# Optimization experiments

Measured on AMD Instinct MI355X. Metric: run time of the kernel, lower is better.

## Reference

```python
import jax, jax.numpy as jnp
import numpy as np

B = 4096          # batch_size * world_size
D = 256           # embedding dim
TEMP = 0.5        # temperature
EPS = 1e-8        # torch CosineSimilarity eps


def setup_inputs() -> dict:
    key = jax.random.key(0)
    k1, k2 = jax.random.split(key)
    z_i = jax.random.normal(k1, (B, D), dtype=jnp.float32)
    z_j = jax.random.normal(k2, (B, D), dtype=jnp.float32)
    return {"z_i": z_i, "z_j": z_j}


def reference(z_i, z_j):
    N = 2 * B
    z = jnp.concatenate([z_i, z_j], axis=0)                      # [N, D]
    # Cosine similarity: normalize rows (clamped norm like torch eps), then matmul.
    norms = jnp.maximum(jnp.linalg.norm(z, axis=1, keepdims=True), EPS)
    zn = z / norms
    sim = jnp.matmul(zn, zn.T) / TEMP                            # [N, N]
    # Positive pairs: offsets +B and -B from the diagonal.
    pos = jnp.concatenate([jnp.diagonal(sim, B), jnp.diagonal(sim, -B)])  # [N]
    # Cross-entropy with label 0 over [pos, negatives]:
    # logsumexp over {pos} U {negatives} == logsumexp over row excluding the diagonal
    # (the (i, i±B) entries removed by the mask are exactly re-added as the positive).
    neg_inf = jnp.array(-jnp.inf, dtype=sim.dtype)
    sim_nodiag = jnp.where(jnp.eye(N, dtype=bool), neg_inf, sim)
    lse = jax.nn.logsumexp(sim_nodiag, axis=1)                   # [N]
    loss = jnp.sum(lse - pos) / N                                # reduction='sum' then /N
    return loss
```

## Files before the change

### kernel.cpp

```cpp
#include <hip/hip_runtime.h>

#define NROWS 8192
#define DIM   256
#define BHALF 4096
#define NCHUNK 8
#define SCALE 1.69864358f
#define LN2F  0.69314718f

typedef unsigned char u8;
typedef __attribute__((ext_vector_type(4))) float f32x4;
typedef __attribute__((ext_vector_type(4))) int   i32x4;
typedef __attribute__((ext_vector_type(8))) int   i32x8;

__device__ inline void gload_lds16(const void* g, void* l) {
  __builtin_amdgcn_global_load_lds(
      (const __attribute__((address_space(1))) void*)g,
      (__attribute__((address_space(3))) void*)l, 16, 0, 0);
}

__device__ inline float fp8_to_f32(int b) {
  const int e = (b >> 3) & 15, m = b & 7;
  float mag = e ? __builtin_bit_cast(float, ((e + 120) << 23) | (m << 20))
                : (float)m * 0x1p-9f;
  return (b & 128) ? -mag : mag;
}

__global__ __launch_bounds__(256) void nrm_kernel(const float* __restrict__ zi,
                                                  const float* __restrict__ zj,
                                                  u8* __restrict__ zn8,
                                                  float* __restrict__ rowsum,
                                                  float* __restrict__ pos,
                                                  float* __restrict__ diag,
                                                  int* __restrict__ cnt,
                                                  float* __restrict__ out) {
  const int t = threadIdx.x, b = blockIdx.x;
  const int gid = b * 256 + t;
  if (gid < NROWS) rowsum[gid] = 0.f;
  if (gid < 64) cnt[gid] = 0;
  if (gid == 0) out[0] = 0.f;

  const int w = t >> 6, l = t & 63;
#pragma unroll
  for (int q = 0; q < 2; ++q) {
    const int p = b * 8 + w * 2 + q;
    float4 vi = *(const float4*)(zi + (size_t)p * DIM + l * 4);
    float4 vj = *(const float4*)(zj + (size_t)p * DIM + l * 4);
    float ssi = vi.x * vi.x + vi.y * vi.y + vi.z * vi.z + vi.w * vi.w;
    float ssj = vj.x * vj.x + vj.y * vj.y + vj.z * vj.z + vj.w * vj.w;
#pragma unroll
    for (int m = 1; m < 64; m <<= 1) {
      ssi += __shfl_xor(ssi, m);
      ssj += __shfl_xor(ssj, m);
    }
    const float invi = SCALE / fmaxf(sqrtf(ssi), 1e-8f);
    const float invj = SCALE / fmaxf(sqrtf(ssj), 1e-8f);
    int pi = __builtin_amdgcn_cvt_pk_fp8_f32(vi.x * invi, vi.y * invi, 0, false);
    pi = __builtin_amdgcn_cvt_pk_fp8_f32(vi.z * invi, vi.w * invi, pi, true);
    int pj = __builtin_amdgcn_cvt_pk_fp8_f32(vj.x * invj, vj.y * invj, 0, false);
    pj = __builtin_amdgcn_cvt_pk_fp8_f32(vj.z * invj, vj.w * invj, pj, true);
    *(int*)(zn8 + (size_t)p * DIM + l * 4) = pi;
    *(int*)(zn8 + (size_t)(p + BHALF) * DIM + l * 4) = pj;

    float dot = 0.f, di = 0.f, dj = 0.f;
#pragma unroll
    for (int k2 = 0; k2 < 4; ++k2) {
      const float qi = fp8_to_f32((pi >> (8 * k2)) & 255);
      const float qj = fp8_to_f32((pj >> (8 * k2)) & 255);
      dot += qi * qj; di += qi * qi; dj += qj * qj;
    }
#pragma unroll
    for (int m = 1; m < 64; m <<= 1) {
      dot += __shfl_xor(dot, m);
      di  += __shfl_xor(di, m);
      dj  += __shfl_xor(dj, m);
    }
    if      (l == 0) pos[p] = dot * LN2F;
    else if (l == 1) pos[p + BHALF] = dot * LN2F;
    else if (l == 2) diag[p] = di;
    else if (l == 3) diag[p + BHALF] = dj;
  }
}

__global__ __launch_bounds__(256, 2) void sim_kernel(const u8* __restrict__ zn8,
                                                     float* __restrict__ rowsum,
                                                     const float* __restrict__ pos,
                                                     const float* __restrict__ diag,
                                                     int* __restrict__ cnt,
                                                     float* __restrict__ out) {
  __shared__ __align__(16) u8 Bsm[2][128 * DIM];
  __shared__ float plane[2][128];
  __shared__ float wsum[2];
  __shared__ int sfin;

  const int t = threadIdx.x;
  const int w = t >> 6, l = t & 63;
  const int wa = w >> 1, wb = w & 1;
  const int rl = l & 15, kg = l >> 4;

  const int rp = (int)blockIdx.x >> 3;
  const int ch = (int)blockIdx.x & 7;
  const int colbase = ch * 1024;

  int soff[8], doff[8];
#pragma unroll
  for (int i = 0; i < 8; ++i) {
    int c = i * 256 + t;
    int r = c >> 4, cd = c & 15;
    int cs = (cd & 8) | ((cd ^ r) & 7);
    soff[i] = r * DIM + cs * 16;
    doff[i] = (i * 256 + w * 64) * 16;
  }
  auto STAGE = [&](int base_row, u8* dst) {
#pragma unroll
    for (int i = 0; i < 8; ++i)
      gload_lds16(zn8 + (size_t)base_row * DIM + soff[i], dst + doff[i]);
  };
  auto RD2 = [&](const u8* buf, int row, i32x8* dst) {
    const int salt = row & 7;
    const u8* base = buf + row * DIM;
#pragma unroll
    for (int k = 0; k < 2; ++k) {
      i32x4 lo = *(const i32x4*)(base + ((k * 8 + ((kg * 2) ^ salt)) << 4));
      i32x4 hi = *(const i32x4*)(base + ((k * 8 + ((kg * 2 + 1) ^ salt)) << 4));
      dst[k] = __builtin_shufflevector(lo, hi, 0, 1, 2, 3, 4, 5, 6, 7);
    }
  };

  STAGE(rp * 128, &Bsm[0][0]);
  STAGE(colbase, &Bsm[1][0]);
  asm volatile("s_waitcnt vmcnt(8)" ::: "memory");
  __builtin_amdgcn_sched_barrier(0);
  __builtin_amdgcn_s_barrier();
  __builtin_amdgcn_sched_barrier(0);

  i32x8 pb[4][2];
#pragma unroll
  for (int pj = 0; pj < 4; ++pj)
    RD2(&Bsm[0][0], wb * 64 + pj * 16 + rl, pb[pj]);
  asm volatile("s_waitcnt lgkmcnt(0)" ::: "memory");
  __builtin_amdgcn_sched_barrier(0);

  float rsum[4] = {0.f, 0.f, 0.f, 0.f};
  const f32x4 z4 = {0.f, 0.f, 0.f, 0.f};

  auto EPI = [&](const f32x4* a) {
#pragma unroll
    for (int pj = 0; pj < 4; ++pj)
#pragma unroll
      for (int jj = 0; jj < 4; ++jj)
        rsum[pj] += __builtin_amdgcn_exp2f(a[pj][jj]);
  };

#pragma unroll 2
  for (int ti = 0; ti < 8; ++ti) {
    asm volatile("s_waitcnt vmcnt(0)" ::: "memory");
    __builtin_amdgcn_sched_barrier(0);
    __builtin_amdgcn_s_barrier();
    __builtin_amdgcn_sched_barrier(0);

    const u8* Bb = &Bsm[(ti + 1) & 1][0];
    if (ti < 7) STAGE(colbase + (ti + 1) * 128, &Bsm[ti & 1][0]);

    f32x4 acc[2][4];
    i32x8 af[2][2];
    RD2(Bb, wa * 64 + rl, af[0]);
#pragma unroll
    for (int ci = 0; ci < 4; ++ci) {
      if (ci < 3) RD2(Bb, wa * 64 + (ci + 1) * 16 + rl, af[(ci + 1) & 1]);
      if (ci < 3) asm volatile("s_waitcnt lgkmcnt(4)" ::: "memory");
      else        asm volatile("s_waitcnt lgkmcnt(0)" ::: "memory");
      __builtin_amdgcn_sched_barrier(0);

      __builtin_amdgcn_s_setprio(1);
#pragma unroll
      for (int pj = 0; pj < 4; ++pj)
        acc[ci & 1][pj] = __builtin_amdgcn_mfma_scale_f32_16x16x128_f8f6f4(
            af[ci & 1][0], pb[pj][0], z4,
            0, 0, 0, 0x7f7f7f7f, 0, 0x7f7f7f7f);
#pragma unroll
      for (int pj = 0; pj < 4; ++pj)
        acc[ci & 1][pj] = __builtin_amdgcn_mfma_scale_f32_16x16x128_f8f6f4(
            af[ci & 1][1], pb[pj][1], acc[ci & 1][pj],
            0, 0, 0, 0x7f7f7f7f, 0, 0x7f7f7f7f);
      __builtin_amdgcn_s_setprio(0);
      __builtin_amdgcn_sched_barrier(0);

      if (ci > 0) EPI(acc[(ci - 1) & 1]);
    }
    EPI(acc[1]);
  }

#pragma unroll
  for (int pj = 0; pj < 4; ++pj) {
    rsum[pj] += __shfl_xor(rsum[pj], 16);
    rsum[pj] += __shfl_xor(rsum[pj], 32);
  }
  if (kg == 0) {
#pragma unroll
    for (int pj = 0; pj < 4; ++pj)
      plane[wa][wb * 64 + pj * 16 + rl] = rsum[pj];
  }
  __syncthreads();

  if (t < 128)
    atomicAdd(&rowsum[rp * 128 + t], plane[0][t] + plane[1][t]);
  asm volatile("s_waitcnt vmcnt(0)" ::: "memory");
  __syncthreads();
  if (t == 0) sfin = (atomicAdd(&cnt[rp], 1) == NCHUNK - 1);
  __syncthreads();
  if (sfin) {
    float v = 0.f;
    if (t < 128) {
      const int r = rp * 128 + t;
      float s = atomicAdd(&rowsum[r], 0.f);
      v = logf(s - __builtin_amdgcn_exp2f(diag[r])) - pos[r];
    }
#pragma unroll
    for (int m = 1; m < 64; m <<= 1) v += __shfl_xor(v, m);
    if (l == 0 && t < 128) wsum[w] = v;
    __syncthreads();
    if (t == 0) atomicAdd(out, (wsum[0] + wsum[1]) * (1.f / NROWS));
  }
}

extern "C" void kernel_launch(void* const* d_in, const int* in_sizes, int n_in,
                              void* d_out, int out_size, void* d_ws, size_t ws_size,
                              hipStream_t stream) {
  const float* zi = (const float*)d_in[0];
  const float* zj = (const float*)d_in[1];

  u8*    zn8    = (u8*)d_ws;
  float* rowsum = (float*)((char*)d_ws + (size_t)NROWS * DIM);
  float* pos    = (float*)((char*)rowsum + (size_t)NROWS * 4);
  float* diag   = (float*)((char*)pos + (size_t)NROWS * 4);
  int*   cnt    = (int*)((char*)diag + (size_t)NROWS * 4);
  float* out    = (float*)d_out;

  nrm_kernel<<<512, 256, 0, stream>>>(zi, zj, zn8, rowsum, pos, diag, cnt, out);
  sim_kernel<<<64 * NCHUNK, 256, 0, stream>>>(zn8, rowsum, pos, diag, cnt, out);
}
```

Measured before the change: 31.81 us.

## Switch sim kernel to 32x32x64 FP8 MFMA with per-wave full row ownership

Replaces the 16x16x128 scaled FP8 MFMA tiling, where each wave owned a 64x64 quadrant, with 32x32x64 MFMAs. Each wave now owns 32 column rows against all 128 pinned rows, kept in registers as 16 fragments. The exp2 epilogue moves after the full K loop instead of overlapping with the next MFMA group, and the final per-row reduction now sums over four wave planes. This aims for higher MFMA efficiency and fewer LDS reads of the streaming operand, at the cost of more registers (16 pinned fragments plus 64 accumulators) and losing the overlap of epilogue with compute.

```diff
diff --git a/kernel.cpp b/kernel.cpp
--- a/kernel.cpp
+++ b/kernel.cpp
@@ -8,7 +8,7 @@
 #define LN2F  0.69314718f
 
 typedef unsigned char u8;
-typedef __attribute__((ext_vector_type(4))) float f32x4;
+typedef __attribute__((ext_vector_type(16))) float f32x16;
 typedef __attribute__((ext_vector_type(4))) int   i32x4;
 typedef __attribute__((ext_vector_type(8))) int   i32x8;
 
@@ -88,14 +88,13 @@
                                                      int* __restrict__ cnt,
                                                      float* __restrict__ out) {
   __shared__ __align__(16) u8 Bsm[2][128 * DIM];
-  __shared__ float plane[2][128];
+  __shared__ float plane[4][128];
   __shared__ float wsum[2];
   __shared__ int sfin;
 
   const int t = threadIdx.x;
   const int w = t >> 6, l = t & 63;
-  const int wa = w >> 1, wb = w & 1;
-  const int rl = l & 15, kg = l >> 4;
+  const int n31 = l & 31, kh = l >> 5;
 
   const int rp = (int)blockIdx.x >> 3;
   const int ch = (int)blockIdx.x & 7;
@@ -115,15 +114,13 @@
     for (int i = 0; i < 8; ++i)
       gload_lds16(zn8 + (size_t)base_row * DIM + soff[i], dst + doff[i]);
   };
-  auto RD2 = [&](const u8* buf, int row, i32x8* dst) {
+  auto RD32 = [&](const u8* buf, int row, int kk) -> i32x8 {
     const int salt = row & 7;
     const u8* base = buf + row * DIM;
-#pragma unroll
-    for (int k = 0; k < 2; ++k) {
-      i32x4 lo = *(const i32x4*)(base + ((k * 8 + ((kg * 2) ^ salt)) << 4));
-      i32x4 hi = *(const i32x4*)(base + ((k * 8 + ((kg * 2 + 1) ^ salt)) << 4));
-      dst[k] = __builtin_shufflevector(lo, hi, 0, 1, 2, 3, 4, 5, 6, 7);
-    }
+    const int c0 = kk * 4 + kh * 2;
+    i32x4 lo = *(const i32x4*)(base + (((c0 & 8) | ((c0 ^ salt) & 7)) << 4));
+    i32x4 hi = *(const i32x4*)(base + ((((c0 + 1) & 8) | (((c0 + 1) ^ salt) & 7)) << 4));
+    return __builtin_shufflevector(lo, hi, 0, 1, 2, 3, 4, 5, 6, 7);
   };
 
   STAGE(rp * 128, &Bsm[0][0]);
@@ -133,23 +130,16 @@
   __builtin_amdgcn_s_barrier();
   __builtin_amdgcn_sched_barrier(0);
 
-  i32x8 pb[4][2];
+  i32x8 pb[4][4];
 #pragma unroll
   for (int pj = 0; pj < 4; ++pj)
-    RD2(&Bsm[0][0], wb * 64 + pj * 16 + rl, pb[pj]);
+#pragma unroll
+    for (int kk = 0; kk < 4; ++kk)
+      pb[pj][kk] = RD32(&Bsm[0][0], pj * 32 + n31, kk);
   asm volatile("s_waitcnt lgkmcnt(0)" ::: "memory");
   __builtin_amdgcn_sched_barrier(0);
 
   float rsum[4] = {0.f, 0.f, 0.f, 0.f};
-  const f32x4 z4 = {0.f, 0.f, 0.f, 0.f};
-
-  auto EPI = [&](const f32x4* a) {
-#pragma unroll
-    for (int pj = 0; pj < 4; ++pj)
-#pragma unroll
-      for (int jj = 0; jj < 4; ++jj)
-        rsum[pj] += __builtin_amdgcn_exp2f(a[pj][jj]);
-  };
 
 #pragma unroll 2
   for (int ti = 0; ti < 8; ++ti) {
@@ -161,49 +151,58 @@
     const u8* Bb = &Bsm[(ti + 1) & 1][0];
     if (ti < 7) STAGE(colbase + (ti + 1) * 128, &Bsm[ti & 1][0]);
 
-    f32x4 acc[2][4];
-    i32x8 af[2][2];
-    RD2(Bb, wa * 64 + rl, af[0]);
-#pragma unroll
-    for (int ci = 0; ci < 4; ++ci) {
-      if (ci < 3) RD2(Bb, wa * 64 + (ci + 1) * 16 + rl, af[(ci + 1) & 1]);
-      if (ci < 3) asm volatile("s_waitcnt lgkmcnt(4)" ::: "memory");
-      else        asm volatile("s_waitcnt lgkmcnt(0)" ::: "memory");
+    f32x16 acc[4];
+#pragma unroll
+    for (int pj = 0; pj < 4; ++pj) acc[pj] = (f32x16)(0.f);
+
+    i32x8 af0 = RD32(Bb, w * 32 + n31, 0);
+    i32x8 af1;
+#pragma unroll
+    for (int kk = 0; kk < 4; ++kk) {
+      if (kk < 3) {
+        i32x8 nxt = RD32(Bb, w * 32 + n31, kk + 1);
+        if (kk & 1) af0 = nxt; else af1 = nxt;
+        asm volatile("s_waitcnt lgkmcnt(2)" ::: "memory");
+      } else {
+        asm volatile("s_waitcnt lgkmcnt(0)" ::: "memory");
+      }
       __builtin_amdgcn_sched_barrier(0);
-
+      const i32x8 a = (kk & 1) ? af1 : af0;
       __builtin_amdgcn_s_setprio(1);
 #pragma unroll
       for (int pj = 0; pj < 4; ++pj)
-        acc[ci & 1][pj] = __builtin_amdgcn_mfma_scale_f32_16x16x128_f8f6f4(
-            af[ci & 1][0], pb[pj][0], z4,
-            0, 0, 0, 0x7f7f7f7f, 0, 0x7f7f7f7f);
-#pragma unroll
-      for (int pj = 0; pj < 4; ++pj)
-        acc[ci & 1][pj] = __builtin_amdgcn_mfma_scale_f32_16x16x128_f8f6f4(
-            af[ci & 1][1], pb[pj][1], acc[ci & 1][pj],
-            0, 0, 0, 0x7f7f7f7f, 0, 0x7f7f7f7f);
+        acc[pj] = __builtin_amdgcn_mfma_scale_f32_32x32x64_f8f6f4(
+            a, pb[pj][kk], acc[pj],
+            0, 0,
+            0, 0x7f7f7f7f,
+            0, 0x7f7f7f7f);
       __builtin_amdgcn_s_setprio(0);
-      __builtin_amdgcn_sched_barrier(0);
-
-      if (ci > 0) EPI(acc[(ci - 1) & 1]);
-    }
-    EPI(acc[1]);
+    }
+
+#pragma unroll
+    for (int pj = 0; pj < 4; ++pj) {
+      float e0 = 0.f, e1 = 0.f, e2 = 0.f, e3 = 0.f;
+#pragma unroll
+      for (int r16 = 0; r16 < 16; r16 += 4) {
+        e0 += __builtin_amdgcn_exp2f(acc[pj][r16]);
+        e1 += __builtin_amdgcn_exp2f(acc[pj][r16 + 1]);
+        e2 += __builtin_amdgcn_exp2f(acc[pj][r16 + 2]);
+        e3 += __builtin_amdgcn_exp2f(acc[pj][r16 + 3]);
+      }
+      rsum[pj] += (e0 + e1) + (e2 + e3);
+    }
   }
 
 #pragma unroll
   for (int pj = 0; pj < 4; ++pj) {
-    rsum[pj] += __shfl_xor(rsum[pj], 16);
     rsum[pj] += __shfl_xor(rsum[pj], 32);
-  }
-  if (kg == 0) {
-#pragma unroll
-    for (int pj = 0; pj < 4; ++pj)
-      plane[wa][wb * 64 + pj * 16 + rl] = rsum[pj];
+    if (l < 32) plane[w][pj * 32 + l] = rsum[pj];
   }
   __syncthreads();
 
   if (t < 128)
-    atomicAdd(&rowsum[rp * 128 + t], plane[0][t] + plane[1][t]);
+    atomicAdd(&rowsum[rp * 128 + t],
+              (plane[0][t] + plane[1][t]) + (plane[2][t] + plane[3][t]));
   asm volatile("s_waitcnt vmcnt(0)" ::: "memory");
   __syncthreads();
   if (t == 0) sfin = (atomicAdd(&cnt[rp], 1) == NCHUNK - 1);
```

Result: no change. 31.71 us (-0.3%).

## Drop LDS staging; load column fragments directly from global into registers

Applied to the files above, without the earlier changes.

The sim kernel no longer stages 128-row tiles into shared memory with global_load_lds and barriers. Each wave now reads its MFMA operand fragments straight from global memory (L2/L1) into registers and prefetches the next tile's fragment right after issuing the current MFMAs. This removes the LDS traffic, the swizzle and the per-tile block barriers. The cost is redundant global loads across waves, more VGPRs for the prefetch buffers, and exposed global latency that only the register double-buffering covers.

```diff
diff --git a/kernel.cpp b/kernel.cpp
--- a/kernel.cpp
+++ b/kernel.cpp
@@ -11,12 +11,6 @@
 typedef __attribute__((ext_vector_type(4))) float f32x4;
 typedef __attribute__((ext_vector_type(4))) int   i32x4;
 typedef __attribute__((ext_vector_type(8))) int   i32x8;
-
-__device__ inline void gload_lds16(const void* g, void* l) {
-  __builtin_amdgcn_global_load_lds(
-      (const __attribute__((address_space(1))) void*)g,
-      (__attribute__((address_space(3))) void*)l, 16, 0, 0);
-}
 
 __device__ inline float fp8_to_f32(int b) {
   const int e = (b >> 3) & 15, m = b & 7;
@@ -87,7 +81,6 @@
                                                      const float* __restrict__ diag,
                                                      int* __restrict__ cnt,
                                                      float* __restrict__ out) {
-  __shared__ __align__(16) u8 Bsm[2][128 * DIM];
   __shared__ float plane[2][128];
   __shared__ float wsum[2];
   __shared__ int sfin;
@@ -101,93 +94,64 @@
   const int ch = (int)blockIdx.x & 7;
   const int colbase = ch * 1024;
 
-  int soff[8], doff[8];
-#pragma unroll
-  for (int i = 0; i < 8; ++i) {
-    int c = i * 256 + t;
-    int r = c >> 4, cd = c & 15;
-    int cs = (cd & 8) | ((cd ^ r) & 7);
-    soff[i] = r * DIM + cs * 16;
-    doff[i] = (i * 256 + w * 64) * 16;
-  }
-  auto STAGE = [&](int base_row, u8* dst) {
-#pragma unroll
-    for (int i = 0; i < 8; ++i)
-      gload_lds16(zn8 + (size_t)base_row * DIM + soff[i], dst + doff[i]);
+  auto GRD = [&](int row, i32x4* s) {
+    const u8* base = zn8 + (size_t)row * DIM + kg * 32;
+    s[0] = *(const i32x4*)(base);
+    s[1] = *(const i32x4*)(base + 16);
+    s[2] = *(const i32x4*)(base + 128);
+    s[3] = *(const i32x4*)(base + 144);
   };
-  auto RD2 = [&](const u8* buf, int row, i32x8* dst) {
-    const int salt = row & 7;
-    const u8* base = buf + row * DIM;
-#pragma unroll
-    for (int k = 0; k < 2; ++k) {
-      i32x4 lo = *(const i32x4*)(base + ((k * 8 + ((kg * 2) ^ salt)) << 4));
-      i32x4 hi = *(const i32x4*)(base + ((k * 8 + ((kg * 2 + 1) ^ salt)) << 4));
-      dst[k] = __builtin_shufflevector(lo, hi, 0, 1, 2, 3, 4, 5, 6, 7);
-    }
-  };
-
-  STAGE(rp * 128, &Bsm[0][0]);
-  STAGE(colbase, &Bsm[1][0]);
-  asm volatile("s_waitcnt vmcnt(8)" ::: "memory");
+
+  i32x4 pt[4][4];
+#pragma unroll
+  for (int pj = 0; pj < 4; ++pj)
+    GRD(rp * 128 + wb * 64 + pj * 16 + rl, pt[pj]);
+  i32x4 af[4][4];
+#pragma unroll
+  for (int ci = 0; ci < 4; ++ci)
+    GRD(colbase + wa * 64 + ci * 16 + rl, af[ci]);
   __builtin_amdgcn_sched_barrier(0);
-  __builtin_amdgcn_s_barrier();
-  __builtin_amdgcn_sched_barrier(0);
 
   i32x8 pb[4][2];
 #pragma unroll
-  for (int pj = 0; pj < 4; ++pj)
-    RD2(&Bsm[0][0], wb * 64 + pj * 16 + rl, pb[pj]);
-  asm volatile("s_waitcnt lgkmcnt(0)" ::: "memory");
-  __builtin_amdgcn_sched_barrier(0);
+  for (int pj = 0; pj < 4; ++pj) {
+    pb[pj][0] = __builtin_shufflevector(pt[pj][0], pt[pj][1], 0, 1, 2, 3, 4, 5, 6, 7);
+    pb[pj][1] = __builtin_shufflevector(pt[pj][2], pt[pj][3], 0, 1, 2, 3, 4, 5, 6, 7);
+  }
 
   float rsum[4] = {0.f, 0.f, 0.f, 0.f};
   const f32x4 z4 = {0.f, 0.f, 0.f, 0.f};
 
-  auto EPI = [&](const f32x4* a) {
-#pragma unroll
-    for (int pj = 0; pj < 4; ++pj)
-#pragma unroll
-      for (int jj = 0; jj < 4; ++jj)
-        rsum[pj] += __builtin_amdgcn_exp2f(a[pj][jj]);
-  };
-
 #pragma unroll 2
   for (int ti = 0; ti < 8; ++ti) {
-    asm volatile("s_waitcnt vmcnt(0)" ::: "memory");
-    __builtin_amdgcn_sched_barrier(0);
-    __builtin_amdgcn_s_barrier();
-    __builtin_amdgcn_sched_barrier(0);
-
-    const u8* Bb = &Bsm[(ti + 1) & 1][0];
-    if (ti < 7) STAGE(colbase + (ti + 1) * 128, &Bsm[ti & 1][0]);
-
-    f32x4 acc[2][4];
-    i32x8 af[2][2];
-    RD2(Bb, wa * 64 + rl, af[0]);
+    const int tn = (ti < 7) ? ti + 1 : 7;
+    const int nbase = colbase + tn * 128 + wa * 64 + rl;
+
 #pragma unroll
     for (int ci = 0; ci < 4; ++ci) {
-      if (ci < 3) RD2(Bb, wa * 64 + (ci + 1) * 16 + rl, af[(ci + 1) & 1]);
-      if (ci < 3) asm volatile("s_waitcnt lgkmcnt(4)" ::: "memory");
-      else        asm volatile("s_waitcnt lgkmcnt(0)" ::: "memory");
+      i32x8 a0 = __builtin_shufflevector(af[ci][0], af[ci][1], 0, 1, 2, 3, 4, 5, 6, 7);
+      i32x8 a1 = __builtin_shufflevector(af[ci][2], af[ci][3], 0, 1, 2, 3, 4, 5, 6, 7);
+      f32x4 acc[4];
+      __builtin_amdgcn_s_setprio(1);
+#pragma unroll
+      for (int pj = 0; pj < 4; ++pj)
+        acc[pj] = __builtin_amdgcn_mfma_scale_f32_16x16x128_f8f6f4(
+            a0, pb[pj][0], z4, 0, 0, 0, 0x7f7f7f7f, 0, 0x7f7f7f7f);
+#pragma unroll
+      for (int pj = 0; pj < 4; ++pj)
+        acc[pj] = __builtin_amdgcn_mfma_scale_f32_16x16x128_f8f6f4(
+            a1, pb[pj][1], acc[pj], 0, 0, 0, 0x7f7f7f7f, 0, 0x7f7f7f7f);
+      __builtin_amdgcn_s_setprio(0);
+
+      GRD(nbase + ci * 16, af[ci]);
       __builtin_amdgcn_sched_barrier(0);
 
-      __builtin_amdgcn_s_setprio(1);
 #pragma unroll
       for (int pj = 0; pj < 4; ++pj)
-        acc[ci & 1][pj] = __builtin_amdgcn_mfma_scale_f32_16x16x128_f8f6f4(
-            af[ci & 1][0], pb[pj][0], z4,
-            0, 0, 0, 0x7f7f7f7f, 0, 0x7f7f7f7f);
-#pragma unroll
-      for (int pj = 0; pj < 4; ++pj)
-        acc[ci & 1][pj] = __builtin_amdgcn_mfma_scale_f32_16x16x128_f8f6f4(
-            af[ci & 1][1], pb[pj][1], acc[ci & 1][pj],
-            0, 0, 0, 0x7f7f7f7f, 0, 0x7f7f7f7f);
-      __builtin_amdgcn_s_setprio(0);
-      __builtin_amdgcn_sched_barrier(0);
-
-      if (ci > 0) EPI(acc[(ci - 1) & 1]);
-    }
-    EPI(acc[1]);
+#pragma unroll
+        for (int jj = 0; jj < 4; ++jj)
+          rsum[pj] += __builtin_amdgcn_exp2f(acc[pj][jj]);
+    }
   }
 
 #pragma unroll
```

Result: slower. 49.80 us (+56.6%).
